# Optimization experiments

Hardware: AMD Instinct MI355X
Metric: run time of the kernel (lower is better)

Reference implementation:

```python
import jax, jax.numpy as jnp
import numpy as np

B, S, D, H = 8, 1024, 768, 12
C = D // H          # per-head channels (n_channels)
F = 3072            # MLP hidden nodes
LN_EPS = 1e-5


def _ln(x, g, b):
    m = jnp.mean(x, axis=-1, keepdims=True)
    v = jnp.var(x, axis=-1, keepdims=True)
    return (x - m) / jnp.sqrt(v + LN_EPS) * g + b


def setup_inputs() -> dict:
    key = jax.random.key(0)
    ks = jax.random.split(key, 12)
    w = lambda k, shape: jax.random.normal(k, shape, jnp.float32) * 0.02
    return {
        "x": jax.random.normal(ks[0], (B, S, D), jnp.float32),
        "ln_g": jnp.ones((D,), jnp.float32),
        "ln_b": jnp.zeros((D,), jnp.float32),
        # stacked per-head Q/K/V projections: [H, C_in, C_out]
        "Wq": w(ks[1], (H, C, C)), "bq": jnp.zeros((H, C), jnp.float32),
        "Wk": w(ks[2], (H, C, C)), "bk": jnp.zeros((H, C), jnp.float32),
        "Wv": w(ks[3], (H, C, C)), "bv": jnp.zeros((H, C), jnp.float32),
        # MLP: first (D->F), middle (F->F), last (F->D)
        "W1": w(ks[4], (D, F)), "b1": jnp.zeros((F,), jnp.float32),
        "Wm": w(ks[5], (F, F)), "bm": jnp.zeros((F,), jnp.float32),
        "W2": w(ks[6], (F, D)), "b2": jnp.zeros((D,), jnp.float32),
    }


def reference(x, ln_g, ln_b, Wq, bq, Wk, bk, Wv, bv, W1, b1, Wm, bm, W2, b2):
    b, s, d = x.shape
    h, c = Wq.shape[0], Wq.shape[2]
    # pre-norm (same LayerNorm params reused twice, as in the source)
    n1 = _ln(x, ln_g, ln_b)
    # split features into heads: [b, s, h, c]
    xh = n1.reshape(b, s, h, c)
    q = jnp.einsum('bshd,hdc->bhsc', xh, Wq) + bq[None, :, None, :]
    k = jnp.einsum('bshd,hdc->bhsc', xh, Wk) + bk[None, :, None, :]
    v = jnp.einsum('bshd,hdc->bhsc', xh, Wv) + bv[None, :, None, :]
    scores = jnp.einsum('bhsc,bhtc->bhst', q, k) / jnp.sqrt(jnp.asarray(c, q.dtype))
    p = jax.nn.softmax(scores, axis=-1)
    o = jnp.einsum('bhst,bhtc->bhsc', p, v)
    attn = jnp.transpose(o, (0, 2, 1, 3)).reshape(b, s, d)  # concat heads
    middle = x + attn
    n2 = _ln(middle, ln_g, ln_b)
    # MLP (dropout=0.2 in train; identity at inference): first->act->middle->act->last
    hdn = jax.nn.gelu(n2 @ W1 + b1, approximate=False)
    hdn = jax.nn.gelu(hdn @ Wm + bm, approximate=False)
    mlp_out = hdn @ W2 + b2
    return middle + mlp_out
```

## Files before the change

kernel.cpp:

```cpp
#include <hip/hip_runtime.h>
#include <hip/hip_bf16.h>
#include <cmath>
#include <cstdint>

#define B_ 8
#define S_ 1024
#define D_ 768
#define H_ 12
#define C_ 64
#define F_ 3072
#define NR (B_*S_)
#define LN_EPS 1e-5f

typedef unsigned short u16;
typedef float  f32x4  __attribute__((ext_vector_type(4)));
typedef short  bf16x8 __attribute__((ext_vector_type(8)));

__device__ __forceinline__ u16 f2bf(float f){
  __hip_bfloat16 h = __float2bfloat16(f);
  return *reinterpret_cast<u16*>(&h);
}

__device__ __forceinline__ void gload16(const void* g, void* l){
  __builtin_amdgcn_global_load_lds(
      (const __attribute__((address_space(1))) void*)g,
      (__attribute__((address_space(3))) void*)l, 16, 0, 0);
}

__device__ __forceinline__ void blk_reduce2(float& s, float& sq, float* red){
  #pragma unroll
  for (int o = 32; o > 0; o >>= 1){
    s  += __shfl_down(s,  o, 64);
    sq += __shfl_down(sq, o, 64);
  }
  int w = threadIdx.x >> 6;
  if ((threadIdx.x & 63) == 0){ red[w] = s; red[4+w] = sq; }
  __syncthreads();
  s  = red[0]+red[1]+red[2]+red[3];
  sq = red[4]+red[5]+red[6]+red[7];
}

__global__ __launch_bounds__(256) void ln_kernel(const float* __restrict__ x,
    const float* __restrict__ g, const float* __restrict__ b,
    u16* __restrict__ n1){
  int row = blockIdx.x;
  size_t base = (size_t)row * D_;
  __shared__ float red[8];
  float v[3], s = 0.f, sq = 0.f;
  #pragma unroll
  for (int i = 0; i < 3; i++){
    int j = threadIdx.x + i*256;
    float t = x[base + j];
    v[i] = t; s += t; sq += t*t;
  }
  blk_reduce2(s, sq, red);
  float mean = s * (1.f/D_);
  float var  = sq * (1.f/D_) - mean*mean;
  float rstd = rsqrtf(var + LN_EPS);
  #pragma unroll
  for (int i = 0; i < 3; i++){
    int j = threadIdx.x + i*256;
    n1[base + j] = f2bf((v[i]-mean)*rstd*g[j] + b[j]);
  }
}

__global__ __launch_bounds__(256) void midln_kernel(const float* __restrict__ x,
    const float* __restrict__ attn, const float* __restrict__ g,
    const float* __restrict__ b, float* __restrict__ mid, u16* __restrict__ n2){
  int row = blockIdx.x;
  size_t base = (size_t)row * D_;
  __shared__ float red[8];
  float v[3], s = 0.f, sq = 0.f;
  #pragma unroll
  for (int i = 0; i < 3; i++){
    int j = threadIdx.x + i*256;
    float t = x[base + j] + attn[base + j];
    mid[base + j] = t;
    v[i] = t; s += t; sq += t*t;
  }
  blk_reduce2(s, sq, red);
  float mean = s * (1.f/D_);
  float var  = sq * (1.f/D_) - mean*mean;
  float rstd = rsqrtf(var + LN_EPS);
  #pragma unroll
  for (int i = 0; i < 3; i++){
    int j = threadIdx.x + i*256;
    n2[base + j] = f2bf((v[i]-mean)*rstd*g[j] + b[j]);
  }
}

__global__ void transpose_cast(const float* __restrict__ W, u16* __restrict__ Wt,
                               int K, int N){
  __shared__ float t[32][33];
  int n0 = blockIdx.x*32, k0 = blockIdx.y*32;
  for (int i = threadIdx.y; i < 32; i += 8)
    t[i][threadIdx.x] = W[(size_t)(k0+i)*N + n0 + threadIdx.x];
  __syncthreads();
  for (int i = threadIdx.y; i < 32; i += 8)
    Wt[(size_t)(n0+i)*K + k0 + threadIdx.x] = f2bf(t[threadIdx.x][i]);
}

__global__ __launch_bounds__(256) void qkv_kernel(const u16* __restrict__ n1,
    const float* __restrict__ Wq, const float* __restrict__ bq,
    const float* __restrict__ Wk, const float* __restrict__ bk,
    const float* __restrict__ Wv, const float* __restrict__ bv,
    u16* __restrict__ q, u16* __restrict__ k, u16* __restrict__ v){
  int rt = blockIdx.x;
  int h  = blockIdx.y;
  int tid = threadIdx.x, lane = tid & 63, wid = tid >> 6;
  __shared__ __align__(16) u16 Xs[4096];
  __shared__ __align__(16) u16 Ws[3*4096];

  #pragma unroll
  for (int mat = 0; mat < 3; mat++){
    const float* Wh = (mat==0?Wq:(mat==1?Wk:Wv)) + (size_t)h*4096;
    for (int e = 0; e < 16; e++){
      int flat = e*256 + tid;
      int d = flat >> 6, c = flat & 63;
      Ws[mat*4096 + (d>>3)*512 + c*8 + (d&7)] = f2bf(Wh[flat]);
    }
  }
  for (int r = 0; r < 2; r++){
    int u0 = (r*4 + wid)*64;
    int u = u0 + lane, kc = u >> 6, m = u & 63;
    gload16(n1 + (size_t)(rt*64 + m)*D_ + h*64 + kc*8, &Xs[u0*8]);
  }
  __syncthreads();

  f32x4 acc[4][3];
  #pragma unroll
  for (int mi=0; mi<4; mi++)
    #pragma unroll
    for (int ni=0; ni<3; ni++) acc[mi][ni] = (f32x4){0.f,0.f,0.f,0.f};

  #pragma unroll
  for (int ks = 0; ks < 2; ks++){
    int kc = ks*4 + (lane >> 4);
    bf16x8 a[4], bfr[3];
    #pragma unroll
    for (int mi=0; mi<4; mi++)
      a[mi] = *(const bf16x8*)&Xs[kc*512 + (mi*16 + (lane&15))*8];
    #pragma unroll
    for (int ni=0; ni<3; ni++){
      int co = wid*48 + ni*16 + (lane&15);
      int mat = co >> 6, c = co & 63;
      bfr[ni] = *(const bf16x8*)&Ws[mat*4096 + kc*512 + c*8];
    }
    #pragma unroll
    for (int mi=0; mi<4; mi++)
      #pragma unroll
      for (int ni=0; ni<3; ni++)
        acc[mi][ni] = __builtin_amdgcn_mfma_f32_16x16x32_bf16(a[mi], bfr[ni], acc[mi][ni], 0,0,0);
  }

  #pragma unroll
  for (int ni=0; ni<3; ni++){
    int co = wid*48 + ni*16 + (lane&15);
    int mat = co >> 6, c = co & 63;
    u16* outp = mat==0 ? q : (mat==1 ? k : v);
    const float* bias = mat==0 ? bq : (mat==1 ? bk : bv);
    float bb = bias[h*64 + c];
    #pragma unroll
    for (int mi=0; mi<4; mi++){
      #pragma unroll
      for (int r=0; r<4; r++){
        int grow = rt*64 + mi*16 + (lane>>4)*4 + r;
        int b_ = grow >> 10, s = grow & 1023;
        outp[(((size_t)b_*H_ + h)*S_ + s)*C_ + c] = f2bf(acc[mi][ni][r] + bb);
      }
    }
  }
}

__global__ __launch_bounds__(256) void attn_kernel(const u16* __restrict__ q,
    const u16* __restrict__ k, const u16* __restrict__ v, float* __restrict__ attn){
  int qt = blockIdx.x, bh = blockIdx.y;
  int tid = threadIdx.x, lane = tid & 63, wid = tid >> 6;
  __shared__ __align__(16) u16 Qs[4096], Ks[4096], Vt[4096], Ps[4096];
  const u16* qh = q + (size_t)bh*S_*C_;
  const u16* kh = k + (size_t)bh*S_*C_;
  const u16* vh = v + (size_t)bh*S_*C_;

  for (int r = 0; r < 2; r++){
    int u0 = (r*4 + wid)*64;
    int u = u0 + lane, kc = u >> 6, m = u & 63;
    gload16(qh + (size_t)(qt*64 + m)*C_ + kc*8, &Qs[u0*8]);
  }

  f32x4 o[4];
  #pragma unroll
  for (int ci=0; ci<4; ci++) o[ci] = (f32x4){0.f,0.f,0.f,0.f};
  float mrow[4] = {-1e30f,-1e30f,-1e30f,-1e30f};
  float lrow[4] = {0.f,0.f,0.f,0.f};

  for (int kt = 0; kt < S_/64; kt++){
    __syncthreads();
    for (int r = 0; r < 2; r++){
      int u0 = (r*4 + wid)*64;
      int u = u0 + lane, kc = u >> 6, m = u & 63;
      gload16(kh + (size_t)(kt*64 + m)*C_ + kc*8, &Ks[u0*8]);
    }
    for (int i = 0; i < 2; i++){
      int cc = i*256 + tid;
      int kk2 = cc >> 3, c0 = (cc & 7)*8;
      bf16x8 vv8 = *(const bf16x8*)&vh[(size_t)(kt*64 + kk2)*C_ + c0];
      #pragma unroll
      for (int j = 0; j < 8; j++)
        Vt[(kk2>>3)*512 + (c0+j)*8 + (kk2&7)] = ((const u16*)&vv8)[j];
    }
    __syncthreads();

    f32x4 sfr[4];
    #pragma unroll
    for (int ni=0; ni<4; ni++) sfr[ni] = (f32x4){0.f,0.f,0.f,0.f};
    #pragma unroll
    for (int ks = 0; ks < 2; ks++){
      int kc = ks*4 + (lane >> 4);
      bf16x8 afr = *(const bf16x8*)&Qs[kc*512 + (wid*16 + (lane&15))*8];
      #pragma unroll
      for (int ni=0; ni<4; ni++){
        bf16x8 bfr = *(const bf16x8*)&Ks[kc*512 + (ni*16 + (lane&15))*8];
        sfr[ni] = __builtin_amdgcn_mfma_f32_16x16x32_bf16(afr, bfr, sfr[ni], 0,0,0);
      }
    }

    float alpha[4];
    #pragma unroll
    for (int r = 0; r < 4; r++){
      float mx = -1e30f;
      #pragma unroll
      for (int ni=0; ni<4; ni++){ sfr[ni][r] *= 0.125f; mx = fmaxf(mx, sfr[ni][r]); }
      #pragma unroll
      for (int off = 1; off < 16; off <<= 1) mx = fmaxf(mx, __shfl_xor(mx, off, 64));
      float mnew = fmaxf(mrow[r], mx);
      alpha[r] = __expf(mrow[r] - mnew);
      mrow[r] = mnew;
      float rs = 0.f;
      #pragma unroll
      for (int ni=0; ni<4; ni++){
        float p = __expf(sfr[ni][r] - mnew);
        sfr[ni][r] = p; rs += p;
      }
      #pragma unroll
      for (int off = 1; off < 16; off <<= 1) rs += __shfl_xor(rs, off, 64);
      lrow[r] = lrow[r]*alpha[r] + rs;
    }
    #pragma unroll
    for (int ci=0; ci<4; ci++)
      #pragma unroll
      for (int r=0; r<4; r++) o[ci][r] *= alpha[r];

    #pragma unroll
    for (int ni=0; ni<4; ni++){
      int kcol = ni*16 + (lane&15);
      int kc = kcol >> 3, krm = kcol & 7;
      #pragma unroll
      for (int r=0; r<4; r++){
        int qrow = wid*16 + (lane>>4)*4 + r;
        Ps[kc*512 + qrow*8 + krm] = f2bf(sfr[ni][r]);
      }
    }
    #pragma unroll
    for (int ks = 0; ks < 2; ks++){
      int kc = ks*4 + (lane >> 4);
      bf16x8 afr = *(const bf16x8*)&Ps[kc*512 + (wid*16 + (lane&15))*8];
      #pragma unroll
      for (int ci=0; ci<4; ci++){
        bf16x8 bfr = *(const bf16x8*)&Vt[kc*512 + (ci*16 + (lane&15))*8];
        o[ci] = __builtin_amdgcn_mfma_f32_16x16x32_bf16(afr, bfr, o[ci], 0,0,0);
      }
    }
  }

  int b_ = bh / H_, h = bh % H_;
  #pragma unroll
  for (int ci=0; ci<4; ci++){
    int d = h*64 + ci*16 + (lane&15);
    #pragma unroll
    for (int r=0; r<4; r++){
      int srow = qt*64 + wid*16 + (lane>>4)*4 + r;
      attn[((size_t)b_*S_ + srow)*D_ + d] = o[ci][r] / lrow[r];
    }
  }
}

template<int EPI>
__global__ __launch_bounds__(256) void gemm_kernel(
    const u16* __restrict__ A, const u16* __restrict__ Bt,
    const float* __restrict__ bias, void* __restrict__ outp,
    const float* __restrict__ addin, int M, int N, int K){
  __shared__ __align__(16) u16 As[4096], Bs[4096];
  int lane = threadIdx.x & 63, wid = threadIdx.x >> 6;
  int bn = blockIdx.x, bm = blockIdx.y;
  const u16* Ab = A  + (size_t)bm*128*K;
  const u16* Bb = Bt + (size_t)bn*128*K;
  int wm = wid >> 1, wn = wid & 1;
  f32x4 acc[4][4];
  #pragma unroll
  for (int mi=0; mi<4; mi++)
    #pragma unroll
    for (int ni=0; ni<4; ni++) acc[mi][ni] = (f32x4){0.f,0.f,0.f,0.f};

  for (int kt = 0; kt < K/32; kt++){
    for (int r = 0; r < 2; r++){
      int u0 = (r*4 + wid)*64;
      int u = u0 + lane, kc = u >> 7, m = u & 127;
      gload16(Ab + (size_t)m*K + kt*32 + kc*8, &As[u0*8]);
      gload16(Bb + (size_t)m*K + kt*32 + kc*8, &Bs[u0*8]);
    }
    __syncthreads();
    bf16x8 a[4], b[4];
    int kc = lane >> 4;
    #pragma unroll
    for (int mi=0; mi<4; mi++)
      a[mi] = *(const bf16x8*)&As[kc*1024 + (wm*64 + mi*16 + (lane&15))*8];
    #pragma unroll
    for (int ni=0; ni<4; ni++)
      b[ni] = *(const bf16x8*)&Bs[kc*1024 + (wn*64 + ni*16 + (lane&15))*8];
    #pragma unroll
    for (int mi=0; mi<4; mi++)
      #pragma unroll
      for (int ni=0; ni<4; ni++)
        acc[mi][ni] = __builtin_amdgcn_mfma_f32_16x16x32_bf16(a[mi], b[ni], acc[mi][ni], 0,0,0);
    __syncthreads();
  }

  int gm0 = bm*128 + wm*64, gn0 = bn*128 + wn*64;
  #pragma unroll
  for (int mi=0; mi<4; mi++){
    #pragma unroll
    for (int ni=0; ni<4; ni++){
      int gn = gn0 + ni*16 + (lane&15);
      float bb = bias[gn];
      #pragma unroll
      for (int r=0; r<4; r++){
        int gm = gm0 + mi*16 + (lane>>4)*4 + r;
        float val = acc[mi][ni][r] + bb;
        if (EPI == 0){
          float ge = 0.5f*val*(1.f + erff(val*0.70710678118f));
          ((u16*)outp)[(size_t)gm*N + gn] = f2bf(ge);
        } else {
          ((float*)outp)[(size_t)gm*N + gn] = val + addin[(size_t)gm*N + gn];
        }
      }
    }
  }
}

extern "C" void kernel_launch(void* const* d_in, const int* in_sizes, int n_in,
                              void* d_out, int out_size, void* d_ws, size_t ws_size,
                              hipStream_t stream) {
  const float* x   = (const float*)d_in[0];
  const float* lng = (const float*)d_in[1];
  const float* lnb = (const float*)d_in[2];
  const float* Wq  = (const float*)d_in[3];
  const float* bq  = (const float*)d_in[4];
  const float* Wk  = (const float*)d_in[5];
  const float* bk  = (const float*)d_in[6];
  const float* Wv  = (const float*)d_in[7];
  const float* bv  = (const float*)d_in[8];
  const float* W1  = (const float*)d_in[9];
  const float* b1  = (const float*)d_in[10];
  const float* Wm  = (const float*)d_in[11];
  const float* bm  = (const float*)d_in[12];
  const float* W2  = (const float*)d_in[13];
  const float* b2  = (const float*)d_in[14];
  float* out = (float*)d_out;

  char* ws = (char*)d_ws;
  const size_t MB = 1024*1024;
  u16*   n1  = (u16*)(ws + 0);
  u16*   qq  = (u16*)(ws + 12*MB);
  u16*   kk  = (u16*)(ws + 24*MB);
  u16*   vv  = (u16*)(ws + 36*MB);
  float* at  = (float*)(ws + 48*MB);
  u16*   h1  = (u16*)(ws + 12*MB);
  u16*   h2  = (u16*)(ws + 72*MB);
  u16*   w1t = (u16*)(ws + 120*MB);
  u16*   wmt = (u16*)(ws + 125*MB);
  u16*   w2t = (u16*)(ws + 144*MB);

  transpose_cast<<<dim3(F_/32, D_/32), dim3(32,8), 0, stream>>>(W1, w1t, D_, F_);
  transpose_cast<<<dim3(F_/32, F_/32), dim3(32,8), 0, stream>>>(Wm, wmt, F_, F_);
  transpose_cast<<<dim3(D_/32, F_/32), dim3(32,8), 0, stream>>>(W2, w2t, F_, D_);

  ln_kernel<<<NR, 256, 0, stream>>>(x, lng, lnb, n1);
  qkv_kernel<<<dim3(NR/64, H_), 256, 0, stream>>>(n1, Wq, bq, Wk, bk, Wv, bv, qq, kk, vv);
  attn_kernel<<<dim3(S_/64, B_*H_), 256, 0, stream>>>(qq, kk, vv, at);
  midln_kernel<<<NR, 256, 0, stream>>>(x, at, lng, lnb, out, n1 );

  gemm_kernel<0><<<dim3(F_/128, NR/128), 256, 0, stream>>>(n1, w1t, b1, h1, nullptr, NR, F_, D_);
  gemm_kernel<0><<<dim3(F_/128, NR/128), 256, 0, stream>>>(h1, wmt, bm, h2, nullptr, NR, F_, F_);
  gemm_kernel<1><<<dim3(D_/128, NR/128), 256, 0, stream>>>(h2, w2t, b2, out, out, NR, D_, F_);
}
```

Before: 878.0 us.

## Rewrite MLP GEMMs with 8-wave double-buffered pipelined loads and XCD swizzle

Replaces the simple 128x128 GEMM, which had one synchronous load per 32-wide K step, with a 512-thread 128x256 tile kernel. It double-buffers 64-wide K tiles in LDS and overlaps async global-to-LDS loads with MFMA through explicit vmcnt waits and barriers. Block IDs are swizzled across groups of 8 and the MFMA phases get a higher scheduling priority. The aim is to hide memory latency and raise MFMA utilisation in the dominant MLP GEMMs. The cost is more LDS per block and fragile hand-tuned wait counts.

```diff
diff --git a/kernel.cpp b/kernel.cpp
--- a/kernel.cpp
+++ b/kernel.cpp
@@ -284,48 +284,91 @@
   }
 }
 
-template<int EPI>
-__global__ __launch_bounds__(256) void gemm_kernel(
+template<int K_, int EPI>
+__global__ __launch_bounds__(512, 2) void gemm8p_kernel(
     const u16* __restrict__ A, const u16* __restrict__ Bt,
     const float* __restrict__ bias, void* __restrict__ outp,
-    const float* __restrict__ addin, int M, int N, int K){
-  __shared__ __align__(16) u16 As[4096], Bs[4096];
-  int lane = threadIdx.x & 63, wid = threadIdx.x >> 6;
-  int bn = blockIdx.x, bm = blockIdx.y;
-  const u16* Ab = A  + (size_t)bm*128*K;
-  const u16* Bb = Bt + (size_t)bn*128*K;
-  int wm = wid >> 1, wn = wid & 1;
+    const float* __restrict__ addin, int N){
+  constexpr int NT = K_/64;
+  __shared__ __align__(16) u16 As[2*8192];
+  __shared__ __align__(16) u16 Bs[2*16384];
+  int tid = threadIdx.x, lane = tid & 63, wid = tid >> 6;
+  int wm = wid >> 2, wn = wid & 3;
+  int nwg = gridDim.x;
+  int bid = blockIdx.x;
+  int swz = (bid & 7)*(nwg >> 3) + (bid >> 3);
+  int bn = swz >> 6, bm = swz & 63;
+  const u16* Ab = A  + (size_t)bm*128*K_;
+  const u16* Bb = Bt + (size_t)bn*256*K_;
+
+  auto stA = [&](int buf, int h, int kt){
+    int u0 = wid*64;
+    int kc0 = h*4 + (u0 >> 7);
+    int m0 = u0 & 127;
+    gload16(Ab + (size_t)(m0+lane)*K_ + kt*64 + kc0*8,
+            &As[buf*8192 + kc0*1024 + m0*8]);
+  };
+  auto stB = [&](int buf, int h, int kt){
+    #pragma unroll
+    for (int r = 0; r < 2; r++){
+      int u0 = r*512 + wid*64;
+      int kc0 = h*4 + (u0 >> 8);
+      int n0 = u0 & 255;
+      gload16(Bb + (size_t)(n0+lane)*K_ + kt*64 + kc0*8,
+              &Bs[buf*16384 + kc0*2048 + n0*8]);
+    }
+  };
+
   f32x4 acc[4][4];
   #pragma unroll
   for (int mi=0; mi<4; mi++)
     #pragma unroll
     for (int ni=0; ni<4; ni++) acc[mi][ni] = (f32x4){0.f,0.f,0.f,0.f};
 
-  for (int kt = 0; kt < K/32; kt++){
-    for (int r = 0; r < 2; r++){
-      int u0 = (r*4 + wid)*64;
-      int u = u0 + lane, kc = u >> 7, m = u & 127;
-      gload16(Ab + (size_t)m*K + kt*32 + kc*8, &As[u0*8]);
-      gload16(Bb + (size_t)m*K + kt*32 + kc*8, &Bs[u0*8]);
-    }
-    __syncthreads();
-    bf16x8 a[4], b[4];
-    int kc = lane >> 4;
-    #pragma unroll
-    for (int mi=0; mi<4; mi++)
-      a[mi] = *(const bf16x8*)&As[kc*1024 + (wm*64 + mi*16 + (lane&15))*8];
-    #pragma unroll
-    for (int ni=0; ni<4; ni++)
-      b[ni] = *(const bf16x8*)&Bs[kc*1024 + (wn*64 + ni*16 + (lane&15))*8];
-    #pragma unroll
-    for (int mi=0; mi<4; mi++)
-      #pragma unroll
-      for (int ni=0; ni<4; ni++)
-        acc[mi][ni] = __builtin_amdgcn_mfma_f32_16x16x32_bf16(a[mi], b[ni], acc[mi][ni], 0,0,0);
-    __syncthreads();
-  }
-
-  int gm0 = bm*128 + wm*64, gn0 = bn*128 + wn*64;
+#define GPHASE(tb, kk, STAGE) do {                                             \
+    int kc_ = (kk)*4 + (lane>>4);                                              \
+    bf16x8 af[4], bfv[4];                                                      \
+    _Pragma("unroll")                                                          \
+    for (int mi=0; mi<4; mi++)                                                 \
+      af[mi] = *(const bf16x8*)&As[(tb)*8192 + kc_*1024 + (wm*64+mi*16+(lane&15))*8]; \
+    _Pragma("unroll")                                                          \
+    for (int ni=0; ni<4; ni++)                                                 \
+      bfv[ni] = *(const bf16x8*)&Bs[(tb)*16384 + kc_*2048 + (wn*64+ni*16+(lane&15))*8]; \
+    STAGE;                                                                     \
+    asm volatile("s_waitcnt vmcnt(6)" ::: "memory");                           \
+    __builtin_amdgcn_s_barrier();                                              \
+    asm volatile("s_waitcnt lgkmcnt(0)" ::: "memory");                         \
+    __builtin_amdgcn_sched_barrier(0);                                         \
+    __builtin_amdgcn_s_setprio(1);                                             \
+    _Pragma("unroll")                                                          \
+    for (int mi=0; mi<4; mi++)                                                 \
+      _Pragma("unroll")                                                        \
+      for (int ni=0; ni<4; ni++)                                               \
+        acc[mi][ni] = __builtin_amdgcn_mfma_f32_16x16x32_bf16(af[mi], bfv[ni], acc[mi][ni], 0,0,0); \
+    __builtin_amdgcn_s_setprio(0);                                             \
+    __builtin_amdgcn_s_barrier();                                              \
+  } while(0)
+
+  stA(0,0,0); stB(0,0,0);
+  stA(0,1,0); stB(0,1,0);
+  stA(1,0,1); stB(1,0,1);
+  asm volatile("s_waitcnt vmcnt(6)" ::: "memory");
+  __builtin_amdgcn_s_barrier();
+
+  for (int i = 0; i < NT/2; i++){
+    int t  = 2*i;
+    int t1 = t+1;
+    int t2 = (t+2 < NT) ? t+2 : NT-1;
+    int t3 = (t+3 < NT) ? t+3 : NT-1;
+    GPHASE(0, 0, { stA(1,1,t1); stB(1,1,t1); });
+    GPHASE(0, 1, { stA(0,0,t2); stB(0,0,t2); });
+    GPHASE(1, 0, { stA(0,1,t2); stB(0,1,t2); });
+    GPHASE(1, 1, { stA(1,0,t3); stB(1,0,t3); });
+  }
+  asm volatile("s_waitcnt vmcnt(0)" ::: "memory");
+#undef GPHASE
+
+  int gm0 = bm*128 + wm*64, gn0 = bn*256 + wn*64;
   #pragma unroll
   for (int mi=0; mi<4; mi++){
     #pragma unroll
@@ -389,7 +432,7 @@
   attn_kernel<<<dim3(S_/64, B_*H_), 256, 0, stream>>>(qq, kk, vv, at);
   midln_kernel<<<NR, 256, 0, stream>>>(x, at, lng, lnb, out, n1 );
 
-  gemm_kernel<0><<<dim3(F_/128, NR/128), 256, 0, stream>>>(n1, w1t, b1, h1, nullptr, NR, F_, D_);
-  gemm_kernel<0><<<dim3(F_/128, NR/128), 256, 0, stream>>>(h1, wmt, bm, h2, nullptr, NR, F_, F_);
-  gemm_kernel<1><<<dim3(D_/128, NR/128), 256, 0, stream>>>(h2, w2t, b2, out, out, NR, D_, F_);
-}
+  gemm8p_kernel<768, 0><<<768, 512, 0, stream>>>(n1, w1t, b1, h1, nullptr, F_);
+  gemm8p_kernel<3072,0><<<768, 512, 0, stream>>>(h1, wmt, bm, h2, nullptr, F_);
+  gemm8p_kernel<3072,1><<<192, 512, 0, stream>>>(h2, w2t, b2, out, out, D_);
+}
```

Result: slower. 934.7 us (+6.5%).

## Replace MLP GEMMs with 256x256 tiled, triple-buffered pipelined kernel

Applied to the files above, without the earlier changes.

Replaces the 128x128 single-buffered GEMM with a 256x256 tile kernel using 512 threads, a three-slot LDS ring prefetched two k-steps ahead with vmcnt waits instead of double __syncthreads, and s_setprio around the MFMA block. Block IDs are remapped per XCD so neighbouring tiles share A and B rows in cache. The goal is to hide global-load latency and raise arithmetic intensity. The cost is more LDS (96KB) and register pressure. The last GEMM gets only 96 blocks, which may underfill the GPU.

```diff
diff --git a/kernel.cpp b/kernel.cpp
--- a/kernel.cpp
+++ b/kernel.cpp
@@ -284,50 +284,75 @@
   }
 }
 
-template<int EPI>
-__global__ __launch_bounds__(256) void gemm_kernel(
+template<int K_, int EPI, int PM, int PN, int PGN>
+__global__ __launch_bounds__(512, 2) void gemm256_kernel(
     const u16* __restrict__ A, const u16* __restrict__ Bt,
     const float* __restrict__ bias, void* __restrict__ outp,
-    const float* __restrict__ addin, int M, int N, int K){
-  __shared__ __align__(16) u16 As[4096], Bs[4096];
-  int lane = threadIdx.x & 63, wid = threadIdx.x >> 6;
-  int bn = blockIdx.x, bm = blockIdx.y;
-  const u16* Ab = A  + (size_t)bm*128*K;
-  const u16* Bb = Bt + (size_t)bn*128*K;
-  int wm = wid >> 1, wn = wid & 1;
-  f32x4 acc[4][4];
-  #pragma unroll
-  for (int mi=0; mi<4; mi++)
+    const float* __restrict__ addin, int N){
+  constexpr int NT = K_/32;
+  __shared__ __align__(16) u16 As[3*8192];
+  __shared__ __align__(16) u16 Bs[3*8192];
+  int tid = threadIdx.x, lane = tid & 63, wid = tid >> 6;
+  int wm = wid >> 2, wn = wid & 3;
+  int bid = blockIdx.x;
+  int j = bid >> 3, xcd = bid & 7;
+  int bm = (xcd/PGN)*PM + (j - (j/PM)*PM);
+  int bn = (xcd - (xcd/PGN)*PGN)*PN + (j/PM);
+  const u16* Ab = A  + (size_t)bm*256*K_;
+  const u16* Bb = Bt + (size_t)bn*256*K_;
+
+  auto stage = [&](int slot, int kt){
+    #pragma unroll
+    for (int r = 0; r < 2; r++){
+      int u0 = r*512 + wid*64;
+      int kc0 = u0 >> 8, m0 = u0 & 255;
+      gload16(Ab + (size_t)(m0+lane)*K_ + kt*32 + kc0*8,
+              &As[slot*8192 + kc0*2048 + m0*8]);
+      gload16(Bb + (size_t)(m0+lane)*K_ + kt*32 + kc0*8,
+              &Bs[slot*8192 + kc0*2048 + m0*8]);
+    }
+  };
+
+  f32x4 acc[8][4];
+  #pragma unroll
+  for (int mi=0; mi<8; mi++)
     #pragma unroll
     for (int ni=0; ni<4; ni++) acc[mi][ni] = (f32x4){0.f,0.f,0.f,0.f};
 
-  for (int kt = 0; kt < K/32; kt++){
-    for (int r = 0; r < 2; r++){
-      int u0 = (r*4 + wid)*64;
-      int u = u0 + lane, kc = u >> 7, m = u & 127;
-      gload16(Ab + (size_t)m*K + kt*32 + kc*8, &As[u0*8]);
-      gload16(Bb + (size_t)m*K + kt*32 + kc*8, &Bs[u0*8]);
-    }
-    __syncthreads();
-    bf16x8 a[4], b[4];
+  stage(0, 0); stage(1, 1);
+  asm volatile("s_waitcnt vmcnt(4)" ::: "memory");
+  __builtin_amdgcn_s_barrier();
+
+  for (int k = 0; k < NT; k++){
+    int slot = k - (k/3)*3;
+    int snx  = (k+2) - ((k+2)/3)*3;
+    int ksrc = (k+2 < NT) ? (k+2) : (NT-1);
+    stage(snx, ksrc);
+
+    bf16x8 af[8], bfv[4];
     int kc = lane >> 4;
     #pragma unroll
-    for (int mi=0; mi<4; mi++)
-      a[mi] = *(const bf16x8*)&As[kc*1024 + (wm*64 + mi*16 + (lane&15))*8];
+    for (int mi=0; mi<8; mi++)
+      af[mi] = *(const bf16x8*)&As[slot*8192 + kc*2048 + (wm*128 + mi*16 + (lane&15))*8];
     #pragma unroll
     for (int ni=0; ni<4; ni++)
-      b[ni] = *(const bf16x8*)&Bs[kc*1024 + (wn*64 + ni*16 + (lane&15))*8];
-    #pragma unroll
-    for (int mi=0; mi<4; mi++)
+      bfv[ni] = *(const bf16x8*)&Bs[slot*8192 + kc*2048 + (wn*64 + ni*16 + (lane&15))*8];
+    asm volatile("s_waitcnt lgkmcnt(0)" ::: "memory");
+    __builtin_amdgcn_sched_barrier(0);
+    __builtin_amdgcn_s_setprio(1);
+    #pragma unroll
+    for (int mi=0; mi<8; mi++)
       #pragma unroll
       for (int ni=0; ni<4; ni++)
-        acc[mi][ni] = __builtin_amdgcn_mfma_f32_16x16x32_bf16(a[mi], b[ni], acc[mi][ni], 0,0,0);
-    __syncthreads();
-  }
-
-  int gm0 = bm*128 + wm*64, gn0 = bn*128 + wn*64;
-  #pragma unroll
-  for (int mi=0; mi<4; mi++){
+        acc[mi][ni] = __builtin_amdgcn_mfma_f32_16x16x32_bf16(af[mi], bfv[ni], acc[mi][ni], 0,0,0);
+    __builtin_amdgcn_s_setprio(0);
+    asm volatile("s_waitcnt vmcnt(4)" ::: "memory");
+    __builtin_amdgcn_s_barrier();
+  }
+
+  int gm0 = bm*256 + wm*128, gn0 = bn*256 + wn*64;
+  #pragma unroll
+  for (int mi=0; mi<8; mi++){
     #pragma unroll
     for (int ni=0; ni<4; ni++){
       int gn = gn0 + ni*16 + (lane&15);
@@ -389,7 +414,7 @@
   attn_kernel<<<dim3(S_/64, B_*H_), 256, 0, stream>>>(qq, kk, vv, at);
   midln_kernel<<<NR, 256, 0, stream>>>(x, at, lng, lnb, out, n1 );
 
-  gemm_kernel<0><<<dim3(F_/128, NR/128), 256, 0, stream>>>(n1, w1t, b1, h1, nullptr, NR, F_, D_);
-  gemm_kernel<0><<<dim3(F_/128, NR/128), 256, 0, stream>>>(h1, wmt, bm, h2, nullptr, NR, F_, F_);
-  gemm_kernel<1><<<dim3(D_/128, NR/128), 256, 0, stream>>>(h2, w2t, b2, out, out, NR, D_, F_);
-}
+  gemm256_kernel<768, 0, 8, 6, 2><<<384, 512, 0, stream>>>(n1, w1t, b1, h1, nullptr, F_);
+  gemm256_kernel<3072,0, 8, 6, 2><<<384, 512, 0, stream>>>(h1, wmt, bm, h2, nullptr, F_);
+  gemm256_kernel<3072,1, 4, 3, 1><<<96,  512, 0, stream>>>(h2, w2t, b2, out, out, D_);
+}
```

Measured after the change: 1.031 ms. 1.17x slower.
